# Kernel tuning notes

Hardware: AMD Instinct MI355X
Metric: run time of the kernel (lower is better)

The kernel has to match this reference:

```python
import jax, jax.numpy as jnp
import numpy as np

# --- static config / quantization scales (simulating the torch-int modules) ---
B, S, E, H = 2, 2048, 2048, 16
D = E // H  # head_dim = 128
CATTN_ALPHA = 0.004   # W8A8B8O8Conv1D requant scale: int32 acc -> int8 out
QK_ALPHA = 1e-4       # BMM_S8T_S8N_F32T: s_q * s_k dequant scale -> fp32 logits
PV_ALPHA = 0.002      # BMM_S8T_S8N_S8T: (1/127)*s_v/s_out requant scale -> int8 out
PROJ_ALPHA = 0.003    # W8A8BFP32OFP32Conv1D dequant scale -> fp32 out


def q8(x):
    """round + saturate to int8 range (values kept in float32)."""
    return jnp.clip(jnp.round(x), -128.0, 127.0)


def setup_inputs() -> dict:
    key = jax.random.key(0)
    k0, k1, k2, k3, k4 = jax.random.split(key, 5)
    i8 = lambda k, shape: jax.random.randint(k, shape, -128, 128).astype(jnp.float32)
    return {
        "hidden_states": i8(k0, (B, S, E)),      # int8 activations (simulated)
        "w_attn": i8(k1, (E, 3 * E)),            # int8 c_attn weight (Conv1D: x @ W)
        "b_attn": i8(k2, (3 * E,)),              # int8 c_attn bias
        "w_proj": i8(k3, (E, E)),                # int8 c_proj weight
        "b_proj": jax.random.normal(k4, (E,), dtype=jnp.float32),  # fp32 c_proj bias
    }


def reference(hidden_states, w_attn, b_attn, w_proj, b_proj):
    # c_attn: W8A8B8O8 — int32 accumulate, requantize, add int8 bias, saturate
    qkv = q8(CATTN_ALPHA * jnp.matmul(hidden_states, w_attn) + b_attn)  # [B,S,3E] int8
    q, k, v = jnp.split(qkv, 3, axis=-1)

    def split_heads(t):  # [B,S,E] -> [B,H,S,D]
        return t.reshape(B, S, H, D).transpose(0, 2, 1, 3)

    q, k, v = split_heads(q), split_heads(k), split_heads(v)

    # qk_bmm: BMM_S8T_S8N_F32T -> fp32 logits, then /sqrt(head_dim)
    logits = QK_ALPHA * jnp.einsum("bhqd,bhkd->bhqk", q, k)
    logits = logits / jnp.float32(np.sqrt(D))

    # causal mask (tril bias buffer); masked positions -> dtype min
    causal = jnp.tril(jnp.ones((S, S), dtype=bool))
    mask_value = jnp.finfo(logits.dtype).min
    logits = jnp.where(causal[None, None], logits, mask_value)

    # softmax, then requantize probabilities to int8: round(p * 127)
    p = jax.nn.softmax(logits, axis=-1)
    p_i8 = q8(p * 127.0)  # [B,H,S,S] int8 (simulated)

    # pv_bmm: BMM_S8T_S8N_S8T -> int8 attn output
    attn_out = q8(PV_ALPHA * jnp.einsum("bhqk,bhkd->bhqd", p_i8, v))  # [B,H,S,D]

    # merge heads -> [B,S,E]
    attn_out = attn_out.transpose(0, 2, 1, 3).reshape(B, S, E)

    # c_proj: W8A8BFP32OFP32 — int32 accumulate, dequant to fp32, add fp32 bias
    out = PROJ_ALPHA * jnp.matmul(attn_out, w_proj) + b_proj  # [B,S,E] fp32
    return out
```

## Files before the change

### kernel.cpp

```cpp
#include <hip/hip_runtime.h>
#include <cstdint>
#include <cstddef>


typedef int v4i __attribute__((ext_vector_type(4)));

static constexpr float CATTN_ALPHA = 0.004f;
static constexpr float PV_ALPHA    = 0.002f;
static constexpr float PROJ_ALPHA  = 0.003f;
static constexpr float CE2   = 1.275174308e-05f;
static constexpr float MAGIC = 12582912.0f;

#define GLL16(gp, lp)                                              \
  __builtin_amdgcn_global_load_lds(                                \
      (const __attribute__((address_space(1))) void*)(gp),         \
      (__attribute__((address_space(3))) void*)(lp), 16, 0, 0)

__device__ __forceinline__ float exp2_fast(float x) {
#if __has_builtin(__builtin_amdgcn_exp2f)
  return __builtin_amdgcn_exp2f(x);
#else
  return __builtin_exp2f(x);
#endif
}

__device__ __forceinline__ uint32_t pack4(uint32_t u0, uint32_t u1, uint32_t u2,
                                          uint32_t u3) {
#if __has_builtin(__builtin_amdgcn_perm)
  uint32_t t01 = __builtin_amdgcn_perm(u1, u0, 0x00000400u);
  uint32_t t23 = __builtin_amdgcn_perm(u3, u2, 0x00000400u);
  return __builtin_amdgcn_perm(t23, t01, 0x05040100u);
#else
  return (u0 & 255u) | ((u1 & 255u) << 8) | ((u2 & 255u) << 16) | (u3 << 24);
#endif
}

__device__ __forceinline__ uint32_t rq8(float alpha, int a, float b) {
  float f = __fadd_rn(__fmul_rn(alpha, (float)a), b);
  f = rintf(f);
  f = fminf(fmaxf(f, -128.f), 127.f);
  return (uint32_t)((int)f) & 255u;
}

__global__ __launch_bounds__(256) void quant_kernel(const float* __restrict__ src,
                                                    int8_t* __restrict__ dst, int n4) {
  int i = blockIdx.x * 256 + threadIdx.x;
  if (i >= n4) return;
  float4 v = reinterpret_cast<const float4*>(src)[i];
  int b0 = __float2int_rn(v.x) & 255;
  int b1 = __float2int_rn(v.y) & 255;
  int b2 = __float2int_rn(v.z) & 255;
  int b3 = __float2int_rn(v.w) & 255;
  reinterpret_cast<int*>(dst)[i] = b0 | (b1 << 8) | (b2 << 16) | (b3 << 24);
}

__global__ __launch_bounds__(256) void quant_transpose_kernel(const float* __restrict__ src,
                                                              int8_t* __restrict__ dst,
                                                              int K, int N) {
  __shared__ int8_t ts[64][68];
  const int k0 = blockIdx.x * 64, n0 = blockIdx.y * 64;
  const int t = threadIdx.x;
  for (int c = t; c < 1024; c += 256) {
    int r = c >> 4, cc = (c & 15) << 2;
    float4 v = *reinterpret_cast<const float4*>(&src[(size_t)(k0 + r) * N + n0 + cc]);
    int b0 = __float2int_rn(v.x) & 255;
    int b1 = __float2int_rn(v.y) & 255;
    int b2 = __float2int_rn(v.z) & 255;
    int b3 = __float2int_rn(v.w) & 255;
    *reinterpret_cast<int*>(&ts[r][cc]) = b0 | (b1 << 8) | (b2 << 16) | (b3 << 24);
  }
  __syncthreads();
  {
    int c = t;
    int rn = c >> 2, ck = (c & 3) << 4;
    __attribute__((aligned(16))) int8_t tmp[16];
#pragma unroll
    for (int j = 0; j < 16; ++j) tmp[j] = ts[ck + j][rn];
    *reinterpret_cast<v4i*>(&dst[(size_t)(n0 + rn) * K + k0 + ck]) =
        *reinterpret_cast<const v4i*>(tmp);
  }
}

__global__ __launch_bounds__(256) void gemm_cattn_kernel(
    const int8_t* __restrict__ A, const int8_t* __restrict__ BT,
    const float* __restrict__ bias,
    int8_t* __restrict__ qout, int8_t* __restrict__ kout, int8_t* __restrict__ vtout) {
  __shared__ __align__(16) int8_t As[2][128][128];
  __shared__ __align__(16) int8_t Bs[2][128][128];
  const int t = threadIdx.x;
  const int lane = t & 63, wave = t >> 6;
  const int wr = wave >> 1, wc = wave & 1;
  const int l15 = lane & 15, l4 = lane >> 4;
  const int m0 = blockIdx.y * 128, n0 = blockIdx.x * 128;

  const int srow = lane >> 3;
  const int scol = ((lane & 7) ^ srow) << 4;
  const int8_t* ag = A + (size_t)(m0 + wave * 32 + srow) * 2048 + scol;
  const int8_t* bg = BT + (size_t)(n0 + wave * 32 + srow) * 2048 + scol;

  auto stage = [&](int b, int ki) {
    const int8_t* a_ = ag + ki * 128;
    const int8_t* b_ = bg + ki * 128;
#pragma unroll
    for (int g = 0; g < 4; ++g) {
      GLL16(a_ + (size_t)(g * 8) * 2048, &As[b][wave * 32 + g * 8][0]);
      GLL16(b_ + (size_t)(g * 8) * 2048, &Bs[b][wave * 32 + g * 8][0]);
    }
  };

  v4i acc[4][4];
#pragma unroll
  for (int i = 0; i < 4; ++i)
#pragma unroll
    for (int j = 0; j < 4; ++j) acc[i][j] = (v4i){0, 0, 0, 0};

  const int rswz = (l4 ^ (l15 & 7)) << 4;
  const int aoff = (wr * 64 + l15) * 128 + rswz;
  const int boff = (wc * 64 + l15) * 128 + rswz;
  const int which = n0 >> 11;

  stage(0, 0);
  if (which == 2) {
    for (int ki = 0; ki < 16; ++ki) {
      if (ki < 15) {
        stage((ki + 1) & 1, ki + 1);
        asm volatile("s_waitcnt vmcnt(8)" ::: "memory");
      } else {
        asm volatile("s_waitcnt vmcnt(0)" ::: "memory");
      }
      __builtin_amdgcn_sched_barrier(0);
      __builtin_amdgcn_s_barrier();
      __builtin_amdgcn_sched_barrier(0);
      const int8_t* ab = &As[ki & 1][0][0];
      const int8_t* bb = &Bs[ki & 1][0][0];
#pragma unroll
      for (int ks = 0; ks < 2; ++ks) {
        v4i af[4], bf[4];
#pragma unroll
        for (int i = 0; i < 4; ++i)
          af[i] = *reinterpret_cast<const v4i*>(ab + ((aoff + i * 2048) ^ (ks * 64)));
#pragma unroll
        for (int j = 0; j < 4; ++j)
          bf[j] = *reinterpret_cast<const v4i*>(bb + ((boff + j * 2048) ^ (ks * 64)));
#pragma unroll
        for (int i = 0; i < 4; ++i)
#pragma unroll
          for (int j = 0; j < 4; ++j)
            acc[i][j] = __builtin_amdgcn_mfma_i32_16x16x64_i8(af[i], bf[j], acc[i][j], 0, 0, 0);
      }
      __builtin_amdgcn_sched_barrier(0);
      __builtin_amdgcn_s_barrier();
    }
  } else {
    for (int ki = 0; ki < 16; ++ki) {
      if (ki < 15) {
        stage((ki + 1) & 1, ki + 1);
        asm volatile("s_waitcnt vmcnt(8)" ::: "memory");
      } else {
        asm volatile("s_waitcnt vmcnt(0)" ::: "memory");
      }
      __builtin_amdgcn_sched_barrier(0);
      __builtin_amdgcn_s_barrier();
      __builtin_amdgcn_sched_barrier(0);
      const int8_t* ab = &As[ki & 1][0][0];
      const int8_t* bb = &Bs[ki & 1][0][0];
#pragma unroll
      for (int ks = 0; ks < 2; ++ks) {
        v4i af[4], bf[4];
#pragma unroll
        for (int i = 0; i < 4; ++i)
          af[i] = *reinterpret_cast<const v4i*>(ab + ((aoff + i * 2048) ^ (ks * 64)));
#pragma unroll
        for (int j = 0; j < 4; ++j)
          bf[j] = *reinterpret_cast<const v4i*>(bb + ((boff + j * 2048) ^ (ks * 64)));
#pragma unroll
        for (int i = 0; i < 4; ++i)
#pragma unroll
          for (int j = 0; j < 4; ++j)
            acc[i][j] = __builtin_amdgcn_mfma_i32_16x16x64_i8(bf[j], af[i], acc[i][j], 0, 0, 0);
      }
      __builtin_amdgcn_sched_barrier(0);
      __builtin_amdgcn_s_barrier();
    }
  }

  const int hh = (n0 & 2047) >> 7;
  const int bi = m0 >> 11;
  const int s_base = m0 & 2047;

  if (which == 2) {
    float bv[4];
#pragma unroll
    for (int j = 0; j < 4; ++j) bv[j] = bias[n0 + wc * 64 + j * 16 + l15];
    int8_t* vb = vtout + ((size_t)(bi * 16 + hh) * 128) * 2048;
#pragma unroll
    for (int i = 0; i < 4; ++i) {
#pragma unroll
      for (int j = 0; j < 4; ++j) {
        uint32_t w = pack4(rq8(CATTN_ALPHA, acc[i][j][0], bv[j]),
                           rq8(CATTN_ALPHA, acc[i][j][1], bv[j]),
                           rq8(CATTN_ALPHA, acc[i][j][2], bv[j]),
                           rq8(CATTN_ALPHA, acc[i][j][3], bv[j]));
        int d = wc * 64 + j * 16 + l15;
        int s0i = s_base + wr * 64 + i * 16 + l4 * 4;
        *reinterpret_cast<uint32_t*>(vb + (size_t)d * 2048 + s0i) = w;
      }
    }
  } else {
    int8_t* dst = (which == 0) ? qout : kout;
    int8_t* db = dst + ((size_t)(bi * 16 + hh) * 2048 + s_base) * 128;
#pragma unroll
    for (int j = 0; j < 4; ++j) {
      float4 b4 = *reinterpret_cast<const float4*>(&bias[n0 + wc * 64 + j * 16 + l4 * 4]);
#pragma unroll
      for (int i = 0; i < 4; ++i) {
        uint32_t w = pack4(rq8(CATTN_ALPHA, acc[i][j][0], b4.x),
                           rq8(CATTN_ALPHA, acc[i][j][1], b4.y),
                           rq8(CATTN_ALPHA, acc[i][j][2], b4.z),
                           rq8(CATTN_ALPHA, acc[i][j][3], b4.w));
        int s_loc = wr * 64 + i * 16 + l15;
        int d0 = wc * 64 + j * 16 + l4 * 4;
        *reinterpret_cast<uint32_t*>(db + (size_t)s_loc * 128 + d0) = w;
      }
    }
  }
}

__global__ __launch_bounds__(256) void gemm_cproj_kernel(
    const int8_t* __restrict__ A, const int8_t* __restrict__ BT,
    const float* __restrict__ bias, float* __restrict__ out) {
  __shared__ __align__(16) int8_t As[2][128][128];
  __shared__ __align__(16) int8_t Bs[2][128][128];
  const int t = threadIdx.x;
  const int lane = t & 63, wave = t >> 6;
  const int wr = wave >> 1, wc = wave & 1;
  const int l15 = lane & 15, l4 = lane >> 4;
  const int m0 = blockIdx.y * 128, n0 = blockIdx.x * 128;

  const int srow = lane >> 3;
  const int scol = ((lane & 7) ^ srow) << 4;
  const int8_t* ag = A + (size_t)(m0 + wave * 32 + srow) * 2048 + scol;
  const int8_t* bg = BT + (size_t)(n0 + wave * 32 + srow) * 2048 + scol;

  auto stage = [&](int b, int ki) {
    const int8_t* a_ = ag + ki * 128;
    const int8_t* b_ = bg + ki * 128;
#pragma unroll
    for (int g = 0; g < 4; ++g) {
      GLL16(a_ + (size_t)(g * 8) * 2048, &As[b][wave * 32 + g * 8][0]);
      GLL16(b_ + (size_t)(g * 8) * 2048, &Bs[b][wave * 32 + g * 8][0]);
    }
  };

  v4i acc[4][4];
#pragma unroll
  for (int i = 0; i < 4; ++i)
#pragma unroll
    for (int j = 0; j < 4; ++j) acc[i][j] = (v4i){0, 0, 0, 0};

  const int rswz = (l4 ^ (l15 & 7)) << 4;
  const int aoff = (wr * 64 + l15) * 128 + rswz;
  const int boff = (wc * 64 + l15) * 128 + rswz;

  stage(0, 0);
  for (int ki = 0; ki < 16; ++ki) {
    if (ki < 15) {
      stage((ki + 1) & 1, ki + 1);
      asm volatile("s_waitcnt vmcnt(8)" ::: "memory");
    } else {
      asm volatile("s_waitcnt vmcnt(0)" ::: "memory");
    }
    __builtin_amdgcn_sched_barrier(0);
    __builtin_amdgcn_s_barrier();
    __builtin_amdgcn_sched_barrier(0);
    const int8_t* ab = &As[ki & 1][0][0];
    const int8_t* bb = &Bs[ki & 1][0][0];
#pragma unroll
    for (int ks = 0; ks < 2; ++ks) {
      v4i af[4], bf[4];
#pragma unroll
      for (int i = 0; i < 4; ++i)
        af[i] = *reinterpret_cast<const v4i*>(ab + ((aoff + i * 2048) ^ (ks * 64)));
#pragma unroll
      for (int j = 0; j < 4; ++j)
        bf[j] = *reinterpret_cast<const v4i*>(bb + ((boff + j * 2048) ^ (ks * 64)));
#pragma unroll
      for (int i = 0; i < 4; ++i)
#pragma unroll
        for (int j = 0; j < 4; ++j)
          acc[i][j] = __builtin_amdgcn_mfma_i32_16x16x64_i8(bf[j], af[i], acc[i][j], 0, 0, 0);
    }
    __builtin_amdgcn_sched_barrier(0);
    __builtin_amdgcn_s_barrier();
  }
#pragma unroll
  for (int j = 0; j < 4; ++j) {
    float4 b4 = *reinterpret_cast<const float4*>(&bias[n0 + wc * 64 + j * 16 + l4 * 4]);
#pragma unroll
    for (int i = 0; i < 4; ++i) {
      int m = m0 + wr * 64 + i * 16 + l15;
      int n = n0 + wc * 64 + j * 16 + l4 * 4;
      float4 o;
      o.x = __fadd_rn(__fmul_rn(PROJ_ALPHA, (float)acc[i][j][0]), b4.x);
      o.y = __fadd_rn(__fmul_rn(PROJ_ALPHA, (float)acc[i][j][1]), b4.y);
      o.z = __fadd_rn(__fmul_rn(PROJ_ALPHA, (float)acc[i][j][2]), b4.z);
      o.w = __fadd_rn(__fmul_rn(PROJ_ALPHA, (float)acc[i][j][3]), b4.w);
      *reinterpret_cast<float4*>(&out[(size_t)m * 2048 + n]) = o;
    }
  }
}

__global__ __launch_bounds__(256) void attn_kernel(
    const int8_t* __restrict__ Q, const int8_t* __restrict__ K8,
    const int8_t* __restrict__ VT, int8_t* __restrict__ O) {
  __shared__ __align__(16) int8_t q_s[64][128];
  __shared__ __align__(16) int8_t k_s[2][64][128];
  __shared__ __align__(16) int8_t vt_s[2][128][64];
  __shared__ __align__(16) int8_t p_s[64][80];

  const int t = threadIdx.x;
  const int lane = t & 63, wave = t >> 6;
  const int l15 = lane & 15, l4 = lane >> 4;
  const int bh = blockIdx.x;
  const int qt = (int)gridDim.y - 1 - (int)blockIdx.y;
  const int r0 = qt * 64;
  const size_t kqbase = (size_t)bh * (2048 * 128);
  const size_t vtbase = (size_t)bh * (128 * 2048);

  const int kq_go = ((lane >> 3) << 7) + ((((lane & 7) ^ (lane >> 3)) & 7) << 4);
  const int vt_go = ((lane >> 2) * 2048) + ((lane & 3) << 4);
  const int koff0 = (l15 << 7) + ((((0 + l4) ^ l15) & 7) << 4);
  const int koff1 = (l15 << 7) + ((((4 + l4) ^ l15) & 7) << 4);
  const int voff = l15 * 64 + l4 * 16;
  const int poff_w = (wave * 16 + l15) * 80 + l4 * 4;
  const int poff_r = (wave * 16 + l15) * 80 + l4 * 16;

  {
    const int8_t* qg = Q + kqbase + (size_t)(r0 + wave * 16) * 128 + kq_go;
    GLL16(qg, &q_s[wave * 16][0]);
    GLL16(qg + 8 * 128, &q_s[wave * 16 + 8][0]);
    const int8_t* kg = K8 + kqbase + (size_t)(wave * 16) * 128 + kq_go;
    GLL16(kg, &k_s[0][wave * 16][0]);
    GLL16(kg + 8 * 128, &k_s[0][wave * 16 + 8][0]);
  }
  __syncthreads();

  const v4i qf0 = *reinterpret_cast<const v4i*>(&q_s[0][0] + wave * 2048 + koff0);
  const v4i qf1 = *reinterpret_cast<const v4i*>(&q_s[0][0] + wave * 2048 + koff1);
  const int qgl = wave * 16 + l15;

  float acc_l[4] = {0.f, 0.f, 0.f, 0.f};

  for (int tt = 0; tt <= qt; ++tt) {
    if (tt < qt) {
      const int8_t* kg =
          K8 + kqbase + (size_t)((tt + 1) * 64 + wave * 16) * 128 + kq_go;
      GLL16(kg, &k_s[(tt + 1) & 1][wave * 16][0]);
      GLL16(kg + 8 * 128, &k_s[(tt + 1) & 1][wave * 16 + 8][0]);
    }
    const int8_t* kb = &k_s[tt & 1][0][0];
    v4i sacc[4];
#pragma unroll
    for (int ni = 0; ni < 4; ++ni) sacc[ni] = (v4i){0, 0, 0, 0};
#pragma unroll
    for (int ni = 0; ni < 4; ++ni) {
      v4i ak = *reinterpret_cast<const v4i*>(kb + ni * 2048 + koff0);
      sacc[ni] = __builtin_amdgcn_mfma_i32_16x16x64_i8(ak, qf0, sacc[ni], 0, 0, 0);
    }
#pragma unroll
    for (int ni = 0; ni < 4; ++ni) {
      v4i ak = *reinterpret_cast<const v4i*>(kb + ni * 2048 + koff1);
      sacc[ni] = __builtin_amdgcn_mfma_i32_16x16x64_i8(ak, qf1, sacc[ni], 0, 0, 0);
    }
    if (tt < qt) {
#pragma unroll
      for (int ni = 0; ni < 4; ++ni)
#pragma unroll
        for (int rr = 0; rr < 4; ++rr)
          acc_l[rr] += exp2_fast(CE2 * (float)sacc[ni][rr]);
    } else {
#pragma unroll
      for (int ni = 0; ni < 4; ++ni)
#pragma unroll
        for (int rr = 0; rr < 4; ++rr) {
          float e = exp2_fast(CE2 * (float)sacc[ni][rr]);
          acc_l[rr] += (ni * 16 + l4 * 4 + rr <= qgl) ? e : 0.f;
        }
    }
    __syncthreads();
  }
  float l_run = (acc_l[0] + acc_l[1]) + (acc_l[2] + acc_l[3]);
  l_run += __shfl_xor(l_run, 16);
  l_run += __shfl_xor(l_run, 32);
  const float inv = 127.0f / l_run;

  {
    const int8_t* kg = K8 + kqbase + (size_t)(wave * 16) * 128 + kq_go;
    GLL16(kg, &k_s[0][wave * 16][0]);
    GLL16(kg + 8 * 128, &k_s[0][wave * 16 + 8][0]);
    const int8_t* vg = VT + vtbase + (size_t)(wave * 32) * 2048 + vt_go;
    GLL16(vg, &vt_s[0][wave * 32][0]);
    GLL16(vg + (size_t)16 * 2048, &vt_s[0][wave * 32 + 16][0]);
  }
  __syncthreads();

  v4i oacc[8];
#pragma unroll
  for (int nj = 0; nj < 8; ++nj) oacc[nj] = (v4i){0, 0, 0, 0};

  for (int tt = 0; tt <= qt; ++tt) {
    if (tt < qt) {
      const int kb1 = (tt + 1) * 64;
      const int8_t* kg = K8 + kqbase + (size_t)(kb1 + wave * 16) * 128 + kq_go;
      GLL16(kg, &k_s[(tt + 1) & 1][wave * 16][0]);
      GLL16(kg + 8 * 128, &k_s[(tt + 1) & 1][wave * 16 + 8][0]);
      const int8_t* vg = VT + vtbase + (size_t)(wave * 32) * 2048 + kb1 + vt_go;
      GLL16(vg, &vt_s[(tt + 1) & 1][wave * 32][0]);
      GLL16(vg + (size_t)16 * 2048, &vt_s[(tt + 1) & 1][wave * 32 + 16][0]);
    }
    const int8_t* kb = &k_s[tt & 1][0][0];
    v4i sacc[4];
#pragma unroll
    for (int ni = 0; ni < 4; ++ni) sacc[ni] = (v4i){0, 0, 0, 0};
#pragma unroll
    for (int ni = 0; ni < 4; ++ni) {
      v4i ak = *reinterpret_cast<const v4i*>(kb + ni * 2048 + koff0);
      sacc[ni] = __builtin_amdgcn_mfma_i32_16x16x64_i8(ak, qf0, sacc[ni], 0, 0, 0);
    }
#pragma unroll
    for (int ni = 0; ni < 4; ++ni) {
      v4i ak = *reinterpret_cast<const v4i*>(kb + ni * 2048 + koff1);
      sacc[ni] = __builtin_amdgcn_mfma_i32_16x16x64_i8(ak, qf1, sacc[ni], 0, 0, 0);
    }
    if (tt < qt) {
#pragma unroll
      for (int ni = 0; ni < 4; ++ni) {
        float f0 = fmaf(exp2_fast(CE2 * (float)sacc[ni][0]), inv, MAGIC);
        float f1 = fmaf(exp2_fast(CE2 * (float)sacc[ni][1]), inv, MAGIC);
        float f2 = fmaf(exp2_fast(CE2 * (float)sacc[ni][2]), inv, MAGIC);
        float f3 = fmaf(exp2_fast(CE2 * (float)sacc[ni][3]), inv, MAGIC);
        uint32_t w = pack4(__float_as_uint(f0), __float_as_uint(f1),
                           __float_as_uint(f2), __float_as_uint(f3));
        *reinterpret_cast<uint32_t*>(&p_s[0][0] + poff_w + ni * 16) = w;
      }
    } else {
#pragma unroll
      for (int ni = 0; ni < 4; ++ni) {
        float e0 = exp2_fast(CE2 * (float)sacc[ni][0]);
        float e1 = exp2_fast(CE2 * (float)sacc[ni][1]);
        float e2 = exp2_fast(CE2 * (float)sacc[ni][2]);
        float e3 = exp2_fast(CE2 * (float)sacc[ni][3]);
        int c = ni * 16 + l4 * 4;
        e0 = (c + 0 <= qgl) ? e0 : 0.f;
        e1 = (c + 1 <= qgl) ? e1 : 0.f;
        e2 = (c + 2 <= qgl) ? e2 : 0.f;
        e3 = (c + 3 <= qgl) ? e3 : 0.f;
        float f0 = fmaf(e0, inv, MAGIC), f1 = fmaf(e1, inv, MAGIC);
        float f2 = fmaf(e2, inv, MAGIC), f3 = fmaf(e3, inv, MAGIC);
        uint32_t w = pack4(__float_as_uint(f0), __float_as_uint(f1),
                           __float_as_uint(f2), __float_as_uint(f3));
        *reinterpret_cast<uint32_t*>(&p_s[0][0] + poff_w + ni * 16) = w;
      }
    }
    asm volatile("s_waitcnt lgkmcnt(0)" ::: "memory");
    v4i pf = *reinterpret_cast<const v4i*>(&p_s[0][0] + poff_r);
    const int8_t* vb = &vt_s[tt & 1][0][0];
#pragma unroll
    for (int nj = 0; nj < 8; ++nj) {
      v4i vf = *reinterpret_cast<const v4i*>(vb + nj * 1024 + voff);
      oacc[nj] = __builtin_amdgcn_mfma_i32_16x16x64_i8(vf, pf, oacc[nj], 0, 0, 0);
    }
    __syncthreads();
  }

  const int bq = bh >> 4, hh = bh & 15;
  {
    int r = r0 + wave * 16 + l15;
    int8_t* ob = O + ((size_t)bq * 2048 + r) * 2048 + hh * 128;
#pragma unroll
    for (int nj = 0; nj < 8; ++nj) {
      uint32_t w = pack4(rq8(PV_ALPHA, oacc[nj][0], 0.f),
                         rq8(PV_ALPHA, oacc[nj][1], 0.f),
                         rq8(PV_ALPHA, oacc[nj][2], 0.f),
                         rq8(PV_ALPHA, oacc[nj][3], 0.f));
      *reinterpret_cast<uint32_t*>(ob + nj * 16 + l4 * 4) = w;
    }
  }
}

extern "C" void kernel_launch(void* const* d_in, const int* in_sizes, int n_in,
                              void* d_out, int out_size, void* d_ws, size_t ws_size,
                              hipStream_t stream) {
  const float* hs_f    = (const float*)d_in[0];
  const float* wattn_f = (const float*)d_in[1];
  const float* battn_f = (const float*)d_in[2];
  const float* wproj_f = (const float*)d_in[3];
  const float* bproj_f = (const float*)d_in[4];
  float* out_f = (float*)d_out;

  int8_t* ws = (int8_t*)d_ws;
  int8_t* hs_i8   = ws;
  int8_t* wT_attn = ws + 8388608;
  int8_t* wT_proj = ws + 20971520;
  int8_t* q_i8    = ws + 25165824;
  int8_t* k_i8    = ws + 33554432;
  int8_t* vT_i8   = ws + 41943040;
  int8_t* attn_i8 = ws + 50331648;

  quant_kernel<<<dim3(8192), dim3(256), 0, stream>>>(hs_f, hs_i8, 2097152);
  quant_transpose_kernel<<<dim3(32, 96), dim3(256), 0, stream>>>(wattn_f, wT_attn, 2048, 6144);
  quant_transpose_kernel<<<dim3(32, 32), dim3(256), 0, stream>>>(wproj_f, wT_proj, 2048, 2048);
  gemm_cattn_kernel<<<dim3(48, 32), dim3(256), 0, stream>>>(hs_i8, wT_attn, battn_f,
                                                            q_i8, k_i8, vT_i8);
  attn_kernel<<<dim3(32, 32), dim3(256), 0, stream>>>(q_i8, k_i8, vT_i8, attn_i8);
  gemm_cproj_kernel<<<dim3(16, 32), dim3(256), 0, stream>>>(attn_i8, wT_proj, bproj_f, out_f);
}
```

Measured before the change: 172.1 us.

## Halve c_attn GEMM K-tile and unify MFMA operand order across Q/K/V

The c_attn GEMM now stages 64-wide K slices instead of 128-wide ones, with a new LDS swizzle and 32 pipeline iterations. This halves shared memory per block, which may raise occupancy. The separate Q/K versus V loops, which swapped the MFMA operands, are merged into a single loop. Because the Q/K outputs now come out transposed from the accumulator layout, their epilogue writes individual bytes instead of packed 32-bit words. This trades coalesced stores and per-iteration amortisation of barriers for lower LDS use and simpler code.

```diff
diff --git a/kernel.cpp b/kernel.cpp
--- a/kernel.cpp
+++ b/kernel.cpp
@@ -85,27 +85,26 @@
     const int8_t* __restrict__ A, const int8_t* __restrict__ BT,
     const float* __restrict__ bias,
     int8_t* __restrict__ qout, int8_t* __restrict__ kout, int8_t* __restrict__ vtout) {
-  __shared__ __align__(16) int8_t As[2][128][128];
-  __shared__ __align__(16) int8_t Bs[2][128][128];
+  __shared__ __align__(16) int8_t As[2][128][64];
+  __shared__ __align__(16) int8_t Bs[2][128][64];
   const int t = threadIdx.x;
   const int lane = t & 63, wave = t >> 6;
   const int wr = wave >> 1, wc = wave & 1;
   const int l15 = lane & 15, l4 = lane >> 4;
   const int m0 = blockIdx.y * 128, n0 = blockIdx.x * 128;
 
-  const int srow = lane >> 3;
-  const int scol = ((lane & 7) ^ srow) << 4;
+  const int srow = lane >> 2;
+  const int scol = (((lane & 3) ^ ((lane >> 3) & 3)) << 4);
   const int8_t* ag = A + (size_t)(m0 + wave * 32 + srow) * 2048 + scol;
   const int8_t* bg = BT + (size_t)(n0 + wave * 32 + srow) * 2048 + scol;
 
   auto stage = [&](int b, int ki) {
-    const int8_t* a_ = ag + ki * 128;
-    const int8_t* b_ = bg + ki * 128;
-#pragma unroll
-    for (int g = 0; g < 4; ++g) {
-      GLL16(a_ + (size_t)(g * 8) * 2048, &As[b][wave * 32 + g * 8][0]);
-      GLL16(b_ + (size_t)(g * 8) * 2048, &Bs[b][wave * 32 + g * 8][0]);
-    }
+    const int8_t* a_ = ag + ki * 64;
+    GLL16(a_, &As[b][wave * 32][0]);
+    GLL16(a_ + (size_t)16 * 2048, &As[b][wave * 32 + 16][0]);
+    const int8_t* b_ = bg + ki * 64;
+    GLL16(b_, &Bs[b][wave * 32][0]);
+    GLL16(b_ + (size_t)16 * 2048, &Bs[b][wave * 32 + 16][0]);
   };
 
   v4i acc[4][4];
@@ -114,84 +113,48 @@
 #pragma unroll
     for (int j = 0; j < 4; ++j) acc[i][j] = (v4i){0, 0, 0, 0};
 
-  const int rswz = (l4 ^ (l15 & 7)) << 4;
-  const int aoff = (wr * 64 + l15) * 128 + rswz;
-  const int boff = (wc * 64 + l15) * 128 + rswz;
+  const int rsz = ((l4 ^ ((l15 >> 1) & 3)) << 4);
+  const int aoff = (wr * 64 + l15) * 64 + rsz;
+  const int boff = (wc * 64 + l15) * 64 + rsz;
+
+  stage(0, 0);
+  for (int ki = 0; ki < 32; ++ki) {
+    if (ki < 31) {
+      stage((ki + 1) & 1, ki + 1);
+      asm volatile("s_waitcnt vmcnt(4)" ::: "memory");
+    } else {
+      asm volatile("s_waitcnt vmcnt(0)" ::: "memory");
+    }
+    __builtin_amdgcn_sched_barrier(0);
+    __builtin_amdgcn_s_barrier();
+    __builtin_amdgcn_sched_barrier(0);
+    const int8_t* ab = &As[ki & 1][0][0];
+    const int8_t* bb = &Bs[ki & 1][0][0];
+    v4i af[4], bf[4];
+#pragma unroll
+    for (int i = 0; i < 4; ++i)
+      af[i] = *reinterpret_cast<const v4i*>(ab + aoff + i * 1024);
+#pragma unroll
+    for (int j = 0; j < 4; ++j)
+      bf[j] = *reinterpret_cast<const v4i*>(bb + boff + j * 1024);
+#pragma unroll
+    for (int i = 0; i < 4; ++i)
+#pragma unroll
+      for (int j = 0; j < 4; ++j)
+        acc[i][j] = __builtin_amdgcn_mfma_i32_16x16x64_i8(af[i], bf[j], acc[i][j], 0, 0, 0);
+    __builtin_amdgcn_sched_barrier(0);
+    __builtin_amdgcn_s_barrier();
+  }
+
   const int which = n0 >> 11;
-
-  stage(0, 0);
-  if (which == 2) {
-    for (int ki = 0; ki < 16; ++ki) {
-      if (ki < 15) {
-        stage((ki + 1) & 1, ki + 1);
-        asm volatile("s_waitcnt vmcnt(8)" ::: "memory");
-      } else {
-        asm volatile("s_waitcnt vmcnt(0)" ::: "memory");
-      }
-      __builtin_amdgcn_sched_barrier(0);
-      __builtin_amdgcn_s_barrier();
-      __builtin_amdgcn_sched_barrier(0);
-      const int8_t* ab = &As[ki & 1][0][0];
-      const int8_t* bb = &Bs[ki & 1][0][0];
-#pragma unroll
-      for (int ks = 0; ks < 2; ++ks) {
-        v4i af[4], bf[4];
-#pragma unroll
-        for (int i = 0; i < 4; ++i)
-          af[i] = *reinterpret_cast<const v4i*>(ab + ((aoff + i * 2048) ^ (ks * 64)));
-#pragma unroll
-        for (int j = 0; j < 4; ++j)
-          bf[j] = *reinterpret_cast<const v4i*>(bb + ((boff + j * 2048) ^ (ks * 64)));
-#pragma unroll
-        for (int i = 0; i < 4; ++i)
-#pragma unroll
-          for (int j = 0; j < 4; ++j)
-            acc[i][j] = __builtin_amdgcn_mfma_i32_16x16x64_i8(af[i], bf[j], acc[i][j], 0, 0, 0);
-      }
-      __builtin_amdgcn_sched_barrier(0);
-      __builtin_amdgcn_s_barrier();
-    }
-  } else {
-    for (int ki = 0; ki < 16; ++ki) {
-      if (ki < 15) {
-        stage((ki + 1) & 1, ki + 1);
-        asm volatile("s_waitcnt vmcnt(8)" ::: "memory");
-      } else {
-        asm volatile("s_waitcnt vmcnt(0)" ::: "memory");
-      }
-      __builtin_amdgcn_sched_barrier(0);
-      __builtin_amdgcn_s_barrier();
-      __builtin_amdgcn_sched_barrier(0);
-      const int8_t* ab = &As[ki & 1][0][0];
-      const int8_t* bb = &Bs[ki & 1][0][0];
-#pragma unroll
-      for (int ks = 0; ks < 2; ++ks) {
-        v4i af[4], bf[4];
-#pragma unroll
-        for (int i = 0; i < 4; ++i)
-          af[i] = *reinterpret_cast<const v4i*>(ab + ((aoff + i * 2048) ^ (ks * 64)));
-#pragma unroll
-        for (int j = 0; j < 4; ++j)
-          bf[j] = *reinterpret_cast<const v4i*>(bb + ((boff + j * 2048) ^ (ks * 64)));
-#pragma unroll
-        for (int i = 0; i < 4; ++i)
-#pragma unroll
-          for (int j = 0; j < 4; ++j)
-            acc[i][j] = __builtin_amdgcn_mfma_i32_16x16x64_i8(bf[j], af[i], acc[i][j], 0, 0, 0);
-      }
-      __builtin_amdgcn_sched_barrier(0);
-      __builtin_amdgcn_s_barrier();
-    }
-  }
-
   const int hh = (n0 & 2047) >> 7;
   const int bi = m0 >> 11;
   const int s_base = m0 & 2047;
+  float bv[4];
+#pragma unroll
+  for (int j = 0; j < 4; ++j) bv[j] = bias[n0 + wc * 64 + j * 16 + l15];
 
   if (which == 2) {
-    float bv[4];
-#pragma unroll
-    for (int j = 0; j < 4; ++j) bv[j] = bias[n0 + wc * 64 + j * 16 + l15];
     int8_t* vb = vtout + ((size_t)(bi * 16 + hh) * 128) * 2048;
 #pragma unroll
     for (int i = 0; i < 4; ++i) {
@@ -210,19 +173,18 @@
     int8_t* dst = (which == 0) ? qout : kout;
     int8_t* db = dst + ((size_t)(bi * 16 + hh) * 2048 + s_base) * 128;
 #pragma unroll
-    for (int j = 0; j < 4; ++j) {
-      float4 b4 = *reinterpret_cast<const float4*>(&bias[n0 + wc * 64 + j * 16 + l4 * 4]);
-#pragma unroll
-      for (int i = 0; i < 4; ++i) {
-        uint32_t w = pack4(rq8(CATTN_ALPHA, acc[i][j][0], b4.x),
-                           rq8(CATTN_ALPHA, acc[i][j][1], b4.y),
-                           rq8(CATTN_ALPHA, acc[i][j][2], b4.z),
-                           rq8(CATTN_ALPHA, acc[i][j][3], b4.w));
-        int s_loc = wr * 64 + i * 16 + l15;
-        int d0 = wc * 64 + j * 16 + l4 * 4;
-        *reinterpret_cast<uint32_t*>(db + (size_t)s_loc * 128 + d0) = w;
-      }
-    }
+    for (int i = 0; i < 4; ++i)
+#pragma unroll
+      for (int j = 0; j < 4; ++j)
+#pragma unroll
+        for (int rr = 0; rr < 4; ++rr) {
+          float f = __fadd_rn(__fmul_rn(CATTN_ALPHA, (float)acc[i][j][rr]), bv[j]);
+          f = rintf(f);
+          f = fminf(fmaxf(f, -128.f), 127.f);
+          int mo = wr * 64 + i * 16 + l4 * 4 + rr;
+          int d = wc * 64 + j * 16 + l15;
+          db[(size_t)mo * 128 + d] = (int8_t)(int)f;
+        }
   }
 }
 
```

Measured after the change: 186.3 us. 8.3% more time.
